# Kernel tuning notes

Measured on AMD Instinct MI355X. Metric: run time of the kernel, lower is better.

The kernel has to match this reference:

```python
import jax, jax.numpy as jnp
import numpy as np
from jax import lax

EPS = 1e-4  # BatchNorm eps from the module

def maxpool2x2(x):
    # x: [N, C, H, W] -> 2x2 max pool, stride 2, no padding
    return lax.reduce_window(x, -jnp.inf, lax.max, (1, 1, 2, 2), (1, 1, 2, 2), 'VALID')

def conv_nchw(x, w):
    return lax.conv_general_dilated(x, w, window_strides=(1, 1), padding='VALID',
                                    dimension_numbers=('NCHW', 'OIHW', 'NCHW'))

def setup_inputs() -> dict:
    key = jax.random.key(0)
    ks = jax.random.split(key, 6)
    return {
        'x':       jax.random.normal(ks[0], (8192, 1, 32, 32), dtype=jnp.float32),
        'conv1_w': jax.random.normal(ks[1], (20, 1, 5, 5), dtype=jnp.float32) * 0.1,
        'conv2_w': jax.random.normal(ks[2], (50, 20, 5, 5), dtype=jnp.float32) * 0.1,
        'lin_w':   jax.random.normal(ks[3], (500, 1250), dtype=jnp.float32) * 0.05,
        'fc_w':    jax.random.normal(ks[4], (10, 500), dtype=jnp.float32) * 0.05,
        'fc_b':    jax.random.normal(ks[5], (10,), dtype=jnp.float32) * 0.05,
    }

def reference(x, conv1_w, conv2_w, lin_w, fc_w, fc_b):
    # --- features ---
    # Conv2d(1, 20, k=5, bias=False): [N,1,32,32] -> [N,20,28,28]
    h = conv_nchw(x, conv1_w)
    # BatchNorm2d(20, eps=1e-4, affine=False), training-mode batch stats (biased var)
    mean = jnp.mean(h, axis=(0, 2, 3), keepdims=True)
    var = jnp.var(h, axis=(0, 2, 3), keepdims=True)
    h = (h - mean) * lax.rsqrt(var + EPS)
    # ReLU + MaxPool 2x2: -> [N,20,14,14]
    h = maxpool2x2(jnp.maximum(h, 0.0))
    # Binarize(): sign of activations
    h = jnp.sign(h)
    # Conv2dBinary(20, 50, k=5): XNOR-style conv = conv with sign(W), scaled by
    # per-output-channel alpha = mean(|W|). -> [N,50,10,10]
    alpha2 = jnp.mean(jnp.abs(conv2_w), axis=(1, 2, 3)).reshape(1, -1, 1, 1)
    h = conv_nchw(h, jnp.sign(conv2_w)) * alpha2
    # Hardtanh + MaxPool 2x2: -> [N,50,5,5]
    h = maxpool2x2(jnp.clip(h, -1.0, 1.0))
    # --- dense ---
    h = h.reshape(h.shape[0], -1)  # [N, 1250], channel-major like torch.flatten
    h = jnp.sign(h)
    # LinearBinary(1250, 500): y = x @ sign(W)^T * alpha, alpha = mean(|W|, dim=1)
    alpha_l = jnp.mean(jnp.abs(lin_w), axis=1)  # [500]
    h = (h @ jnp.sign(lin_w).T) * alpha_l
    h = jnp.clip(h, -1.0, 1.0)
    # fc: Linear(500, num_classes)
    return h @ fc_w.T + fc_b
```

## Files before the change

### kernel.cpp

```cpp
#include <hip/hip_runtime.h>
#include <stdint.h>


#define NIMG 8192

typedef __attribute__((ext_vector_type(8))) _Float16 f16x8;
typedef __attribute__((ext_vector_type(16))) float f32x16;


__global__ __launch_bounds__(64) void prep_k(const float* __restrict__ lw,
                                             const float* __restrict__ w2,
                                             unsigned long long* __restrict__ lwp,
                                             float* __restrict__ alpha,
                                             uint32_t* __restrict__ wp2) {
  int b = blockIdx.x, t = threadIdx.x;
  if (b < 500) {
    int j = b;
    float pa = 0.f;
    for (int k = t; k < 1250; k += 64) pa += fabsf(lw[j * 1250 + k]);
    for (int o = 32; o > 0; o >>= 1) pa += __shfl_down(pa, o, 64);
    if (t == 0) alpha[j] = pa / 1250.0f;
    if (t < 20) {
      unsigned long long m = 0;
      int base = j * 1250 + t * 64;
      int lim = 1250 - t * 64; if (lim > 64) lim = 64;
      for (int bb = 0; bb < lim; ++bb)
        if (lw[base + bb] > 0.f) m |= (1ull << bb);
      lwp[j * 20 + t] = m;
    }
  } else {
    int idx = (b - 500) * 64 + t;
    if (idx < 1250) {
      int oc = idx / 25, k = idx % 25;
      uint32_t m = 0;
      for (int ic = 0; ic < 20; ++ic)
        if (w2[(oc * 20 + ic) * 25 + k] > 0.f) m |= (1u << ic);
      wp2[idx] = m;
    }
  }
}

__global__ __launch_bounds__(256) void sumT_k(const float* __restrict__ x,
                                              float* __restrict__ partial) {
  int b = blockIdx.x, t = threadIdx.x;
  const float4* xv = (const float4*)x + (size_t)b * 64 * 256;
  float ax = 0.f, ay = 0.f, az = 0.f, aw = 0.f;
  for (int nn = 0; nn < 64; ++nn) {
    float4 v = xv[nn * 256 + t];
    ax += v.x; ay += v.y; az += v.z; aw += v.w;
  }
  float4 r; r.x = ax; r.y = ay; r.z = az; r.w = aw;
  ((float4*)(partial + (size_t)b * 1024))[t] = r;
}

__global__ __launch_bounds__(256) void mean_k(const float* __restrict__ partial,
                                              const float* __restrict__ w1,
                                              float* __restrict__ mean) {
  __shared__ float Tsh[1024];
  __shared__ double U8[25][8];
  __shared__ double U[25];
  int t = threadIdx.x;
  for (int e = t; e < 1024; e += 256) {
    double s = 0.0;
    for (int b = 0; b < 128; ++b) s += (double)partial[b * 1024 + e];
    Tsh[e] = (float)s;
  }
  __syncthreads();
  if (t < 200) {
    int tap = t >> 3, part = t & 7;
    int ky = tap / 5, kx = tap % 5;
    double s = 0.0;
    for (int p = part * 98; p < part * 98 + 98; ++p) {
      int py = p / 28, px = p % 28;
      s += (double)Tsh[(py + ky) * 32 + px + kx];
    }
    U8[tap][part] = s;
  }
  __syncthreads();
  if (t < 25) {
    double s = 0.0;
    for (int i = 0; i < 8; ++i) s += U8[t][i];
    U[t] = s;
  }
  __syncthreads();
  if (t < 20) {
    double s = 0.0;
    for (int q = 0; q < 25; ++q) s += (double)w1[t * 25 + q] * U[q];
    mean[t] = (float)(s / (8192.0 * 784.0));
  }
}

__device__ inline uint32_t pack_f16_pair(float fv) {
  _Float16 h = (_Float16)fv;
  float rem = fv - (float)h;
  _Float16 l = (_Float16)(rem * 4096.0f);
  uint32_t hb = (uint32_t)__builtin_bit_cast(unsigned short, h);
  uint32_t lb = (uint32_t)__builtin_bit_cast(unsigned short, l);
  return (hb << 16) | lb;
}

__global__ __launch_bounds__(256) void conv1_mfma_k(const float* __restrict__ x,
                                                    const float* __restrict__ w1,
                                                    const float* __restrict__ mean,
                                                    uint32_t* __restrict__ b1p) {
  __shared__ uint32_t ximg[4][1032];
  int tid = threadIdx.x;
  int wave = tid >> 6, lane = tid & 63;
  int n = blockIdx.x * 4 + wave;
  uint32_t* xs = ximg[wave];

  const float4* xin = (const float4*)(x + (size_t)n * 1024);
#pragma unroll
  for (int i = 0; i < 4; ++i) {
    float4 v = xin[i * 64 + lane];
    float fv[4] = {v.x, v.y, v.z, v.w};
#pragma unroll
    for (int e = 0; e < 4; ++e)
      xs[4 * (i * 64 + lane) + e] = pack_f16_pair(fv[e]);
  }

  int bc = lane & 31;
  int khsel = lane >> 5;
  f16x8 Bh[2], Bl[2];
#pragma unroll
  for (int kh = 0; kh < 2; ++kh)
#pragma unroll
    for (int j = 0; j < 8; ++j) {
      int t = kh * 16 + khsel * 8 + j;
      float wv = (bc < 20 && t < 25) ? w1[bc * 25 + t] : 0.f;
      uint32_t pp = pack_f16_pair(wv);
      Bh[kh][j] = __builtin_bit_cast(_Float16, (unsigned short)(pp >> 16));
      Bl[kh][j] = __builtin_bit_cast(_Float16, (unsigned short)(pp & 0xffffu));
    }
  float mv = (bc < 20) ? mean[bc] : 3.0e38f;

  int offs[2][8];
#pragma unroll
  for (int kh = 0; kh < 2; ++kh)
#pragma unroll
    for (int j = 0; j < 8; ++j) {
      int t = kh * 16 + khsel * 8 + j;
      if (t > 24) t = 24;
      offs[kh][j] = (t / 5) * 32 + (t % 5);
    }

  int m = lane & 31;
  const float INV = 1.0f / 4096.0f;

  for (int pp = 0; pp < 14; ++pp) {
    unsigned long long bacc[16];
#pragma unroll
    for (int r = 0; r < 16; ++r) bacc[r] = 0ull;
#pragma unroll
    for (int py2 = 0; py2 < 2; ++py2) {
      int py = 2 * pp + py2;
      int base = py * 32 + m;
      f16x8 Ah[2], Al[2];
#pragma unroll
      for (int kh = 0; kh < 2; ++kh)
#pragma unroll
        for (int j = 0; j < 8; ++j) {
          uint32_t v = xs[base + offs[kh][j]];
          Ah[kh][j] = __builtin_bit_cast(_Float16, (unsigned short)(v >> 16));
          Al[kh][j] = __builtin_bit_cast(_Float16, (unsigned short)(v & 0xffffu));
        }
      f32x16 acc0, acc1;
#pragma unroll
      for (int i = 0; i < 16; ++i) { acc0[i] = 0.f; acc1[i] = 0.f; }
      acc0 = __builtin_amdgcn_mfma_f32_32x32x16_f16(Ah[0], Bh[0], acc0, 0, 0, 0);
      acc0 = __builtin_amdgcn_mfma_f32_32x32x16_f16(Ah[1], Bh[1], acc0, 0, 0, 0);
      acc1 = __builtin_amdgcn_mfma_f32_32x32x16_f16(Ah[0], Bl[0], acc1, 0, 0, 0);
      acc1 = __builtin_amdgcn_mfma_f32_32x32x16_f16(Ah[1], Bl[1], acc1, 0, 0, 0);
      acc1 = __builtin_amdgcn_mfma_f32_32x32x16_f16(Al[0], Bh[0], acc1, 0, 0, 0);
      acc1 = __builtin_amdgcn_mfma_f32_32x32x16_f16(Al[1], Bh[1], acc1, 0, 0, 0);
#pragma unroll
      for (int r = 0; r < 16; ++r)
        bacc[r] |= __ballot((acc0[r] + INV * acc1[r]) > mv);
    }
    uint32_t pm = 0;
#pragma unroll
    for (int pc = 0; pc < 14; ++pc) {
      int px0 = 2 * pc;
      int r0 = (px0 & 3) + 4 * (px0 >> 3);
      int h0 = (px0 >> 2) & 1;
      unsigned long long mm = bacc[r0] | bacc[r0 + 1];
      uint32_t val = (uint32_t)(mm >> (32 * h0));
      if (lane == pc) pm = val;
    }
    if (lane < 14) b1p[(size_t)n * 196 + pp * 14 + lane] = pm;
  }
}

__global__ __launch_bounds__(256) void conv2lin_k(const uint32_t* __restrict__ b1p,
                                                  const uint32_t* __restrict__ wp2,
                                                  const unsigned long long* __restrict__ lwp,
                                                  const float* __restrict__ alpha,
                                                  const float* __restrict__ fcw,
                                                  const float* __restrict__ fcb,
                                                  float* __restrict__ out) {
  __shared__ uint32_t wsh[1250];
  __shared__ uint32_t bm[4][196];
  __shared__ int sumpc[4][100];
  __shared__ signed char s2sh[4][1280];
  __shared__ float hsh[4][512];
  int tid = threadIdx.x;
  int wave = tid >> 6, lane = tid & 63;
  int n = blockIdx.x * 4 + wave;

  for (int i = tid; i < 1250; i += 256) wsh[i] = wp2[i];
#pragma unroll
  for (int rd = 0; rd < 4; ++rd) {
    int idx = rd * 64 + lane;
    if (idx < 196) bm[wave][idx] = b1p[(size_t)n * 196 + idx];
  }
  __syncthreads();

#pragma unroll
  for (int rd = 0; rd < 2; ++rd) {
    int pp = rd * 64 + lane;
    if (pp < 100) {
      int Y = pp / 10, X = pp % 10, s = 0;
#pragma unroll
      for (int ky = 0; ky < 5; ++ky)
#pragma unroll
        for (int kx = 0; kx < 5; ++kx)
          s += __popc(bm[wave][(Y + ky) * 14 + X + kx]);
      sumpc[wave][pp] = s;
    }
  }

#pragma unroll
  for (int rd = 0; rd < 4; ++rd) {
    int unit = rd * 64 + lane;
    if (unit < 250) {
      int oc = unit / 5, r = unit % 5;
      uint32_t w[25];
#pragma unroll
      for (int i = 0; i < 25; ++i) w[i] = wsh[oc * 25 + i];
      for (int pc = 0; pc < 5; ++pc) {
        uint32_t pa[6][6];
#pragma unroll
        for (int rr = 0; rr < 6; ++rr)
#pragma unroll
          for (int cc = 0; cc < 6; ++cc)
            pa[rr][cc] = bm[wave][(2 * r + rr) * 14 + 2 * pc + cc];
        int best = -1000000;
#pragma unroll
        for (int dy = 0; dy < 2; ++dy)
#pragma unroll
          for (int dx = 0; dx < 2; ++dx) {
            int a = 0;
#pragma unroll
            for (int ky = 0; ky < 5; ++ky)
#pragma unroll
              for (int kx = 0; kx < 5; ++kx)
                a += __popc(w[ky * 5 + kx] & pa[dy + ky][dx + kx]);
            a = 2 * a - sumpc[wave][(2 * r + dy) * 10 + 2 * pc + dx];
            if (a > best) best = a;
          }
        s2sh[wave][5 * unit + pc] = (signed char)((best > 0) - (best < 0));
      }
    }
  }
  if (lane < 30) s2sh[wave][1250 + lane] = 0;

  unsigned long long Pm[20], Nm[20];
  int cp = 0, cn = 0;
#pragma unroll
  for (int k = 0; k < 20; ++k) {
    signed char v = s2sh[wave][k * 64 + lane];
    unsigned long long P = __ballot(v > 0);
    unsigned long long N = __ballot(v < 0);
    Pm[k] = P; Nm[k] = N;
    cp += __popcll(P); cn += __popcll(N);
  }

#pragma unroll
  for (int rd = 0; rd < 8; ++rd) {
    int j = rd * 64 + lane;
    float y = 0.f;
    if (j < 500) {
      const ulonglong2* W2 = (const ulonglong2*)(lwp + (size_t)j * 20);
      int a = 0, b = 0;
#pragma unroll
      for (int i = 0; i < 10; ++i) {
        ulonglong2 w2v = W2[i];
        a += __popcll(w2v.x & Pm[2 * i]) + __popcll(w2v.y & Pm[2 * i + 1]);
        b += __popcll(w2v.x & Nm[2 * i]) + __popcll(w2v.y & Nm[2 * i + 1]);
      }
      int dot = 2 * (a - b) - cp + cn;
      y = alpha[j] * (float)dot;
      y = fminf(1.0f, fmaxf(-1.0f, y));
    }
    hsh[wave][rd * 64 + lane] = y;
  }

  float hv[8];
#pragma unroll
  for (int k = 0; k < 8; ++k) hv[k] = hsh[wave][k * 64 + lane];
#pragma unroll
  for (int o = 0; o < 10; ++o) {
    float pa = 0.f;
#pragma unroll
    for (int k = 0; k < 8; ++k) {
      int j = k * 64 + lane;
      if (j < 500) pa += hv[k] * fcw[o * 500 + j];
    }
    for (int off = 32; off > 0; off >>= 1) pa += __shfl_down(pa, off, 64);
    if (lane == 0) out[(size_t)n * 10 + o] = pa + fcb[o];
  }
}

extern "C" void kernel_launch(void* const* d_in, const int* in_sizes, int n_in,
                              void* d_out, int out_size, void* d_ws, size_t ws_size,
                              hipStream_t stream) {
  const float* x   = (const float*)d_in[0];
  const float* w1  = (const float*)d_in[1];
  const float* w2  = (const float*)d_in[2];
  const float* lw  = (const float*)d_in[3];
  const float* fcw = (const float*)d_in[4];
  const float* fcb = (const float*)d_in[5];
  float* out = (float*)d_out;
  char* ws = (char*)d_ws;

  float*    mean  = (float*)(ws + 0);
  uint32_t* wp2   = (uint32_t*)(ws + 128);
  float*    alpha = (float*)(ws + 5632);
  unsigned long long* lwp = (unsigned long long*)(ws + 7680);
  float*    partial = (float*)(ws + 87808);
  uint32_t* b1p   = (uint32_t*)(ws + 612096);

  prep_k<<<520, 64, 0, stream>>>(lw, w2, lwp, alpha, wp2);
  sumT_k<<<128, 256, 0, stream>>>(x, partial);
  mean_k<<<1, 256, 0, stream>>>(partial, w1, mean);
  conv1_mfma_k<<<2048, 256, 0, stream>>>(x, w1, mean, b1p);
  conv2lin_k<<<2048, 256, 0, stream>>>(b1p, wp2, lwp, alpha, fcw, fcb, out);
}
```

Before: 258.9 us.

## Double sumT grid, pack f16 halves directly, and keep dense outputs in registers

```diff
diff --git a/kernel.cpp b/kernel.cpp
--- a/kernel.cpp
+++ b/kernel.cpp
@@ -43,9 +43,9 @@
 __global__ __launch_bounds__(256) void sumT_k(const float* __restrict__ x,
                                               float* __restrict__ partial) {
   int b = blockIdx.x, t = threadIdx.x;
-  const float4* xv = (const float4*)x + (size_t)b * 64 * 256;
+  const float4* xv = (const float4*)x + (size_t)b * 32 * 256;
   float ax = 0.f, ay = 0.f, az = 0.f, aw = 0.f;
-  for (int nn = 0; nn < 64; ++nn) {
+  for (int nn = 0; nn < 32; ++nn) {
     float4 v = xv[nn * 256 + t];
     ax += v.x; ay += v.y; az += v.z; aw += v.w;
   }
@@ -62,7 +62,7 @@
   int t = threadIdx.x;
   for (int e = t; e < 1024; e += 256) {
     double s = 0.0;
-    for (int b = 0; b < 128; ++b) s += (double)partial[b * 1024 + e];
+    for (int b = 0; b < 256; ++b) s += (double)partial[b * 1024 + e];
     Tsh[e] = (float)s;
   }
   __syncthreads();
@@ -134,18 +134,22 @@
     }
   float mv = (bc < 20) ? mean[bc] : 3.0e38f;
 
-  int offs[2][8];
+  int m = lane & 31;
+
+  int aoff[2][8];
 #pragma unroll
   for (int kh = 0; kh < 2; ++kh)
 #pragma unroll
     for (int j = 0; j < 8; ++j) {
       int t = kh * 16 + khsel * 8 + j;
       if (t > 24) t = 24;
-      offs[kh][j] = (t / 5) * 32 + (t % 5);
-    }
-
-  int m = lane & 31;
+      aoff[kh][j] = m + (t / 5) * 32 + (t % 5);
+    }
+
   const float INV = 1.0f / 4096.0f;
+  f32x16 ZERO;
+#pragma unroll
+  for (int i = 0; i < 16; ++i) ZERO[i] = 0.f;
 
   for (int pp = 0; pp < 14; ++pp) {
     unsigned long long bacc[16];
@@ -153,29 +157,39 @@
     for (int r = 0; r < 16; ++r) bacc[r] = 0ull;
 #pragma unroll
     for (int py2 = 0; py2 < 2; ++py2) {
-      int py = 2 * pp + py2;
-      int base = py * 32 + m;
+      int pybase = (2 * pp + py2) * 32;
+      uint32_t raw[16];
+#pragma unroll
+      for (int kh = 0; kh < 2; ++kh)
+#pragma unroll
+        for (int j = 0; j < 8; ++j)
+          raw[kh * 8 + j] = xs[pybase + aoff[kh][j]];
       f16x8 Ah[2], Al[2];
 #pragma unroll
-      for (int kh = 0; kh < 2; ++kh)
-#pragma unroll
-        for (int j = 0; j < 8; ++j) {
-          uint32_t v = xs[base + offs[kh][j]];
-          Ah[kh][j] = __builtin_bit_cast(_Float16, (unsigned short)(v >> 16));
-          Al[kh][j] = __builtin_bit_cast(_Float16, (unsigned short)(v & 0xffffu));
+      for (int kh = 0; kh < 2; ++kh) {
+        uint32_t hw[4], lw2[4];
+#pragma unroll
+        for (int jj = 0; jj < 4; ++jj) {
+          uint32_t v0 = raw[kh * 8 + 2 * jj], v1 = raw[kh * 8 + 2 * jj + 1];
+          hw[jj] = (v1 & 0xFFFF0000u) | (v0 >> 16);
+          lw2[jj] = (v1 << 16) | (v0 & 0xFFFFu);
         }
+        struct U4 { uint32_t a, b, c, d; };
+        U4 hv4 = {hw[0], hw[1], hw[2], hw[3]};
+        U4 lv4 = {lw2[0], lw2[1], lw2[2], lw2[3]};
+        Ah[kh] = __builtin_bit_cast(f16x8, hv4);
+        Al[kh] = __builtin_bit_cast(f16x8, lv4);
+      }
       f32x16 acc0, acc1;
-#pragma unroll
-      for (int i = 0; i < 16; ++i) { acc0[i] = 0.f; acc1[i] = 0.f; }
-      acc0 = __builtin_amdgcn_mfma_f32_32x32x16_f16(Ah[0], Bh[0], acc0, 0, 0, 0);
+      acc0 = __builtin_amdgcn_mfma_f32_32x32x16_f16(Ah[0], Bh[0], ZERO, 0, 0, 0);
       acc0 = __builtin_amdgcn_mfma_f32_32x32x16_f16(Ah[1], Bh[1], acc0, 0, 0, 0);
-      acc1 = __builtin_amdgcn_mfma_f32_32x32x16_f16(Ah[0], Bl[0], acc1, 0, 0, 0);
+      acc1 = __builtin_amdgcn_mfma_f32_32x32x16_f16(Ah[0], Bl[0], ZERO, 0, 0, 0);
       acc1 = __builtin_amdgcn_mfma_f32_32x32x16_f16(Ah[1], Bl[1], acc1, 0, 0, 0);
       acc1 = __builtin_amdgcn_mfma_f32_32x32x16_f16(Al[0], Bh[0], acc1, 0, 0, 0);
       acc1 = __builtin_amdgcn_mfma_f32_32x32x16_f16(Al[1], Bh[1], acc1, 0, 0, 0);
 #pragma unroll
       for (int r = 0; r < 16; ++r)
-        bacc[r] |= __ballot((acc0[r] + INV * acc1[r]) > mv);
+        bacc[r] |= __ballot(fmaf(INV, acc1[r], acc0[r]) > mv);
     }
     uint32_t pm = 0;
 #pragma unroll
@@ -202,7 +216,6 @@
   __shared__ uint32_t bm[4][196];
   __shared__ int sumpc[4][100];
   __shared__ signed char s2sh[4][1280];
-  __shared__ float hsh[4][512];
   int tid = threadIdx.x;
   int wave = tid >> 6, lane = tid & 63;
   int n = blockIdx.x * 4 + wave;
@@ -275,6 +288,7 @@
     cp += __popcll(P); cn += __popcll(N);
   }
 
+  float hv[8];
 #pragma unroll
   for (int rd = 0; rd < 8; ++rd) {
     int j = rd * 64 + lane;
@@ -292,12 +306,9 @@
       y = alpha[j] * (float)dot;
       y = fminf(1.0f, fmaxf(-1.0f, y));
     }
-    hsh[wave][rd * 64 + lane] = y;
-  }
-
-  float hv[8];
-#pragma unroll
-  for (int k = 0; k < 8; ++k) hv[k] = hsh[wave][k * 64 + lane];
+    hv[rd] = y;
+  }
+
 #pragma unroll
   for (int o = 0; o < 10; ++o) {
     float pa = 0.f;
@@ -328,10 +339,10 @@
   float*    alpha = (float*)(ws + 5632);
   unsigned long long* lwp = (unsigned long long*)(ws + 7680);
   float*    partial = (float*)(ws + 87808);
-  uint32_t* b1p   = (uint32_t*)(ws + 612096);
+  uint32_t* b1p   = (uint32_t*)(ws + 1136384);
 
   prep_k<<<520, 64, 0, stream>>>(lw, w2, lwp, alpha, wp2);
-  sumT_k<<<128, 256, 0, stream>>>(x, partial);
+  sumT_k<<<256, 256, 0, stream>>>(x, partial);
   mean_k<<<1, 256, 0, stream>>>(partial, w1, mean);
   conv1_mfma_k<<<2048, 256, 0, stream>>>(x, w1, mean, b1p);
   conv2lin_k<<<2048, 256, 0, stream>>>(b1p, wp2, lwp, alpha, fcw, fcb, out);
```

Result: slower. 371.5 us (+43.5%).
